# Optimization experiments

Hardware: AMD Instinct MI355X
Metric: run time of the kernel (lower is better)

The kernel has to match this reference:

```python
import jax, jax.numpy as jnp
import numpy as np

IN_DIM, HID_DIM, CNV1_DIM, BATCH = 4096, 2048, 1024, 16384


def setup_inputs() -> dict:
    key = jax.random.key(0)
    ks = jax.random.split(key, 12)
    x = jax.random.normal(ks[0], (BATCH, IN_DIM), dtype=jnp.float32)
    mask_ih = jax.random.randint(ks[1], (HID_DIM, IN_DIM), 0, 2).astype(jnp.bool_)
    mask_hc = jax.random.randint(ks[2], (CNV1_DIM, HID_DIM), 0, 2).astype(jnp.bool_)
    # SparseLinear params (Linear-style: weight [out,in], bias [out])
    lim_ih = 1.0 / np.sqrt(IN_DIM)
    w_ih = jax.random.uniform(ks[3], (HID_DIM, IN_DIM), jnp.float32, -lim_ih, lim_ih)
    b_ih = jax.random.uniform(ks[4], (HID_DIM,), jnp.float32, -lim_ih, lim_ih)
    lim_hc = 1.0 / np.sqrt(HID_DIM)
    w_hc = jax.random.uniform(ks[5], (CNV1_DIM, HID_DIM), jnp.float32, -lim_hc, lim_hc)
    b_hc = jax.random.uniform(ks[6], (CNV1_DIM,), jnp.float32, -lim_hc, lim_hc)
    # Conv1d(1,1,2) weights, kaiming_uniform(tanh): gain=5/3, fan_in=2
    bound = (5.0 / 3.0) * np.sqrt(3.0 / 2.0)
    w_c1 = jax.random.uniform(ks[7], (2,), jnp.float32, -bound, bound)
    w_c2 = jax.random.uniform(ks[8], (2,), jnp.float32, -bound, bound)
    lim_c = 1.0 / np.sqrt(2.0)
    b_c1 = jax.random.uniform(ks[9], (), jnp.float32, -lim_c, lim_c)
    b_c2 = jax.random.uniform(ks[10], (), jnp.float32, -lim_c, lim_c)
    return {"x": x, "mask_ih": mask_ih, "mask_hc": mask_hc,
            "w_ih": w_ih, "b_ih": b_ih, "w_hc": w_hc, "b_hc": b_hc,
            "w_c1": w_c1, "b_c1": b_c1, "w_c2": w_c2, "b_c2": b_c2}


def _conv1d_k2s2(x, w, b):
    # Conv1d(1,1,kernel=2,stride=2) on [B, L] == pairwise reshape + dot
    B, L = x.shape
    return jnp.einsum('blk,k->bl', x.reshape(B, L // 2, 2), w) + b


def reference(x, mask_ih, mask_hc, w_ih, b_ih, w_hc, b_hc, w_c1, b_c1, w_c2, b_c2):
    h = jnp.tanh(x @ (w_ih * mask_ih).T + b_ih)            # [B, HID]
    c = jnp.tanh(h @ (w_hc * mask_hc).T + b_hc)            # [B, CNV1]
    y = jnp.tanh(_conv1d_k2s2(c, w_c1, b_c1))              # [B, CNV1/2]
    y = jnp.tanh(_conv1d_k2s2(y, w_c2, b_c2))              # [B, CNV1/4]
    return y
```

## Files before the change

### kernel.cpp

```cpp
#include <hip/hip_runtime.h>
#include <cstdint>
#include <cstddef>

typedef __bf16  bf16x8f __attribute__((ext_vector_type(8)));
typedef unsigned short u16x8 __attribute__((ext_vector_type(8)));
typedef float   f32x16 __attribute__((ext_vector_type(16)));

__device__ __forceinline__ unsigned short f2bf(float f) {
    union { float f; uint32_t u; } c; c.f = f;
    uint32_t u = c.u;
    return (unsigned short)((u + 0x7fffu + ((u >> 16) & 1u)) >> 16);
}

__device__ __forceinline__ float fast_tanh(float x) {
    float e = __builtin_exp2f(2.885390081777927f * x);
    return 1.0f - 2.0f * __builtin_amdgcn_rcpf(e + 1.0f);
}

__device__ __forceinline__ void load16_lds(const void* g, unsigned short* l) {
    __builtin_amdgcn_global_load_lds(
        (const __attribute__((address_space(1))) unsigned int*)g,
        (__attribute__((address_space(3))) unsigned int*)l,
        16, 0, 0);
}

__global__ __launch_bounds__(256)
void detect_mask(const unsigned char* __restrict__ m, int* __restrict__ flag) {
    __shared__ int s_gt1, s_off;
    if (threadIdx.x == 0) { s_gt1 = 0; s_off = 0; }
    __syncthreads();
    int gt1 = 0, off = 0;
    for (int k = threadIdx.x; k < 4096; k += 256) {
        unsigned char b = m[k];
        if (b > 1) gt1 = 1;
        if ((k & 3) && b) off = 1;
    }
    if (gt1) atomicOr(&s_gt1, 1);
    if (off) atomicOr(&s_off, 1);
    __syncthreads();
    if (threadIdx.x == 0) *flag = (!s_gt1 && s_off) ? 1 : 0;
}

__global__ __launch_bounds__(256)
void cast_f32_bf16(const float* __restrict__ in, unsigned short* __restrict__ out, int n) {
    int tid = blockIdx.x * blockDim.x + threadIdx.x;
    int stride = gridDim.x * blockDim.x;
    for (int e = tid * 4; e < n; e += stride * 4) {
        float4 v = *(const float4*)(in + e);
        ushort4 o;
        o.x = f2bf(v.x); o.y = f2bf(v.y); o.z = f2bf(v.z); o.w = f2bf(v.w);
        *(ushort4*)(out + e) = o;
    }
}

__global__ __launch_bounds__(256)
void mask_cast(const float* __restrict__ w, const void* __restrict__ mv,
               const int* __restrict__ flag, unsigned short* __restrict__ out, int n) {
    const bool u8 = (*flag != 0);
    int tid = blockIdx.x * blockDim.x + threadIdx.x;
    int stride = gridDim.x * blockDim.x;
    for (int e = tid * 4; e < n; e += stride * 4) {
        float4 v = *(const float4*)(w + e);
        int m0, m1, m2, m3;
        if (u8) {
            uchar4 mm = *(const uchar4*)((const unsigned char*)mv + e);
            m0 = mm.x; m1 = mm.y; m2 = mm.z; m3 = mm.w;
        } else {
            int4 mm = ((const int4*)mv)[e >> 2];
            m0 = mm.x; m1 = mm.y; m2 = mm.z; m3 = mm.w;
        }
        ushort4 o;
        o.x = m0 ? f2bf(v.x) : (unsigned short)0;
        o.y = m1 ? f2bf(v.y) : (unsigned short)0;
        o.z = m2 ? f2bf(v.z) : (unsigned short)0;
        o.w = m3 ? f2bf(v.w) : (unsigned short)0;
        *(ushort4*)(out + e) = o;
    }
}

template <typename OutT, bool FUSE>
__global__ __launch_bounds__(512, 2)
void gemm256(const unsigned short* __restrict__ A,
             const unsigned short* __restrict__ W,
             const float* __restrict__ bias,
             OutT* __restrict__ out,
             const float* __restrict__ w1, const float* __restrict__ b1,
             const float* __restrict__ w2, const float* __restrict__ b2,
             int N, int K, int lbx) {
    __shared__ __align__(16) unsigned short lds[65536];

    const int t    = threadIdx.x;
    const int lane = t & 63;
    const int wave = t >> 6;
    const int l31  = lane & 31;
    const int lh   = lane >> 5;
    const int wrow = (wave >> 2) * 128;
    const int wcol = (wave & 3) * 64;

    const int id = blockIdx.x;
    const int bx = id & ((1 << lbx) - 1);
    const int by = id >> lbx;
    const int bm = by * 256, bn = bx * 256;

    const char* Au = (const char*)(A + (size_t)bm * K);
    const char* Wu = (const char*)(W + (size_t)bn * K);

    uint32_t aSrc[2], bSrc[2][2];
#pragma unroll
    for (int j = 0; j < 2; ++j) {
        const int u = t + j * 512;
        { const int r = u >> 2, c = u & 3;
          aSrc[j] = (uint32_t)((r * K + ((c ^ (r & 3)) << 3)) * 2); }
        { const int rl = u >> 3, c = u & 7;
#pragma unroll
          for (int Un = 0; Un < 2; ++Un) {
              const int n = (rl & 31) + ((rl >> 5) << 6) + Un * 32;
              bSrc[Un][j] = (uint32_t)((n * K + ((c ^ (n & 7)) << 3)) * 2);
          } }
    }

    int aRow[4];
#pragma unroll
    for (int mt = 0; mt < 4; ++mt) aRow[mt] = (wrow + mt * 32 + l31) * 32;
    int aSwz[2];
#pragma unroll
    for (int j = 0; j < 2; ++j) aSwz[j] = ((j * 2 + lh) ^ (l31 & 3)) << 3;
    int bBase[2];
#pragma unroll
    for (int nt = 0; nt < 2; ++nt)
        bBase[nt] = 16384 + ((((wcol >> 5) + nt) & 1) * 8192)
                  + (((wcol + nt * 32) >> 6) * 2048) + l31 * 64;
    int bSwz[4];
#pragma unroll
    for (int kp = 0; kp < 2; ++kp)
#pragma unroll
        for (int j = 0; j < 2; ++j)
            bSwz[kp * 2 + j] = ((kp * 4 + j * 2 + lh) ^ (l31 & 7)) << 3;

#define STAGE_A(buf, Uk, kB) do {                                              \
    const char* g_ = Au + (kB);                                                \
    unsigned short* l_ = lds + (buf) * 32768 + (Uk) * 8192 + t * 8;            \
    load16_lds(g_ + aSrc[0] + (Uk) * 64, l_);                                  \
    load16_lds(g_ + aSrc[1] + (Uk) * 64, l_ + 4096);                           \
} while (0)

#define STAGE_B(buf, Un, kB) do {                                              \
    const char* g_ = Wu + (kB);                                                \
    unsigned short* l_ = lds + (buf) * 32768 + 16384 + (Un) * 8192 + t * 8;    \
    load16_lds(g_ + bSrc[Un][0], l_);                                          \
    load16_lds(g_ + bSrc[Un][1], l_ + 4096);                                   \
} while (0)

#define BAR    asm volatile("s_barrier" ::: "memory")
#define VM4BAR do { asm volatile("s_waitcnt vmcnt(4)" ::: "memory"); BAR; } while (0)

#define PHASE(buf, nt, kp, STAGE_STMT) do {                                    \
    u16x8 aF[4][2], bF[2];                                                     \
    const unsigned short* Lb_ = lds + (buf) * 32768;                           \
    _Pragma("unroll")                                                          \
    for (int j_ = 0; j_ < 2; ++j_) {                                           \
        _Pragma("unroll")                                                      \
        for (int mt_ = 0; mt_ < 4; ++mt_)                                      \
            aF[mt_][j_] = *(const u16x8*)(Lb_ + (kp) * 8192 + aRow[mt_] + aSwz[j_]); \
        bF[j_] = *(const u16x8*)(Lb_ + bBase[nt] + bSwz[(kp) * 2 + j_]);       \
    }                                                                          \
    STAGE_STMT;                                                                \
    BAR;                                                                       \
    __builtin_amdgcn_s_setprio(1);                                             \
    _Pragma("unroll")                                                          \
    for (int j_ = 0; j_ < 2; ++j_)                                             \
        _Pragma("unroll")                                                      \
        for (int mt_ = 0; mt_ < 4; ++mt_)                                      \
            acc[mt_][nt] = __builtin_amdgcn_mfma_f32_32x32x16_bf16(            \
                __builtin_bit_cast(bf16x8f, aF[mt_][j_]),                      \
                __builtin_bit_cast(bf16x8f, bF[j_]), acc[mt_][nt], 0, 0, 0);   \
    __builtin_amdgcn_s_setprio(0);                                             \
} while (0)

    f32x16 acc[4][2] = {};

    STAGE_A(0, 0, 0); STAGE_A(0, 1, 0); STAGE_B(0, 0, 0); STAGE_B(0, 1, 0);
    STAGE_A(1, 0, 128); STAGE_B(1, 0, 128);
    asm volatile("s_waitcnt vmcnt(4)" ::: "memory");
    BAR;

    const int KB = K * 2;
    const int KL = KB - 128;
    for (int k0 = 0; k0 < KB; k0 += 256) {
        const int kA = k0 + 128;
        int kB1 = k0 + 256; if (kB1 > KL) kB1 = KL;
        int kB2 = k0 + 384; if (kB2 > KL) kB2 = KL;
        PHASE(0, 0, 0, STAGE_A(1, 1, kA));  BAR;
        PHASE(0, 1, 0, STAGE_B(1, 1, kA));  BAR;
        PHASE(0, 0, 1, STAGE_A(0, 0, kB1)); BAR;
        PHASE(0, 1, 1, STAGE_B(0, 0, kB1)); VM4BAR;
        PHASE(1, 0, 0, STAGE_A(0, 1, kB1)); BAR;
        PHASE(1, 1, 0, STAGE_B(0, 1, kB1)); BAR;
        PHASE(1, 0, 1, STAGE_A(1, 0, kB2)); BAR;
        PHASE(1, 1, 1, STAGE_B(1, 0, kB2)); VM4BAR;
    }
    asm volatile("s_waitcnt vmcnt(0)" ::: "memory");

    float w10 = 0, w11 = 0, bb1 = 0, w20 = 0, w21 = 0, bb2 = 0;
    if constexpr (FUSE) {
        w10 = w1[0]; w11 = w1[1]; bb1 = b1[0];
        w20 = w2[0]; w21 = w2[1]; bb2 = b2[0];
    }
#pragma unroll
    for (int nt = 0; nt < 2; ++nt) {
        const int gn = bn + wcol + nt * 32 + l31;
        const float bv = bias[gn];
#pragma unroll
        for (int mt = 0; mt < 4; ++mt) {
#pragma unroll
            for (int reg = 0; reg < 16; ++reg) {
                const int gm = bm + wrow + mt * 32 + (reg & 3) + 8 * (reg >> 2) + 4 * lh;
                float c = fast_tanh(acc[mt][nt][reg] + bv);
                if constexpr (FUSE) {
                    float c1 = __shfl_xor(c, 1);
                    float c2 = __shfl_xor(c, 2);
                    float c3 = __shfl_xor(c, 3);
                    float y10 = fast_tanh(w10 * c  + w11 * c1 + bb1);
                    float y11 = fast_tanh(w10 * c2 + w11 * c3 + bb1);
                    float y   = fast_tanh(w20 * y10 + w21 * y11 + bb2);
                    if ((lane & 3) == 0)
                        out[(size_t)gm * (N >> 2) + (gn >> 2)] = (OutT)y;
                } else {
                    out[(size_t)gm * N + gn] = (OutT)f2bf(c);
                }
            }
        }
    }
#undef STAGE_A
#undef STAGE_B
#undef BAR
#undef VM4BAR
#undef PHASE
}

extern "C" void kernel_launch(void* const* d_in, const int* in_sizes, int n_in,
                              void* d_out, int out_size, void* d_ws, size_t ws_size,
                              hipStream_t stream) {
    constexpr int B   = 16384;
    constexpr int IN  = 4096;
    constexpr int HID = 2048;
    constexpr int CNV = 1024;

    const float* x       = (const float*)d_in[0];
    const void*  mask_ih = d_in[1];
    const void*  mask_hc = d_in[2];
    const float* w_ih    = (const float*)d_in[3];
    const float* b_ih    = (const float*)d_in[4];
    const float* w_hc    = (const float*)d_in[5];
    const float* b_hc    = (const float*)d_in[6];
    const float* w_c1    = (const float*)d_in[7];
    const float* b_c1    = (const float*)d_in[8];
    const float* w_c2    = (const float*)d_in[9];
    const float* b_c2    = (const float*)d_in[10];
    float* out = (float*)d_out;

    char* ws = (char*)d_ws;
    unsigned short* Xb  = (unsigned short*)(ws);
    unsigned short* Wih = (unsigned short*)(ws + 134217728);
    unsigned short* Whc = (unsigned short*)(ws + 150994944);
    unsigned short* Hb  = (unsigned short*)(ws + 155189248);
    int*            flag = (int*)(ws + 222298112);

    detect_mask<<<1, 256, 0, stream>>>((const unsigned char*)mask_ih, flag);

    cast_f32_bf16<<<4096, 256, 0, stream>>>(x, Xb, B * IN);
    mask_cast<<<1024, 256, 0, stream>>>(w_ih, mask_ih, flag, Wih, HID * IN);
    mask_cast<<<256, 256, 0, stream>>>(w_hc, mask_hc, flag, Whc, CNV * HID);

    gemm256<unsigned short, false><<<512, 512, 0, stream>>>(
        Xb, Wih, b_ih, Hb, nullptr, nullptr, nullptr, nullptr, HID, IN, 3);

    gemm256<float, true><<<256, 512, 0, stream>>>(
        Hb, Whc, b_hc, out, w_c1, b_c1, w_c2, b_c2, CNV, HID, 2);
}
```

Measured before the change: 940.6 us.

## Merge GEMM phases to cover both N-tiles, remap blocks, and change LDS swizzle

Each pipeline phase now loads A fragments once and issues MFMAs for both N sub-tiles, halving the phase count per K step and the redundant A LDS reads. Staging is regrouped two loads per phase with a tighter vmcnt wait. Block IDs are remapped so groups of 8 M-tiles share a column for better L2 reuse of weights. The A-tile LDS swizzle now XORs with (row>>1)&3 to reduce bank conflicts. Fewer barriers, but there is higher register pressure and a less deep prefetch.

```diff
diff --git a/kernel.cpp b/kernel.cpp
--- a/kernel.cpp
+++ b/kernel.cpp
@@ -98,8 +98,8 @@
     const int wcol = (wave & 3) * 64;
 
     const int id = blockIdx.x;
-    const int bx = id & ((1 << lbx) - 1);
-    const int by = id >> lbx;
+    const int bx = (id >> 3) & ((1 << lbx) - 1);
+    const int by = (id & 7) | ((id >> (3 + lbx)) << 3);
     const int bm = by * 256, bn = bx * 256;
 
     const char* Au = (const char*)(A + (size_t)bm * K);
@@ -110,7 +110,7 @@
     for (int j = 0; j < 2; ++j) {
         const int u = t + j * 512;
         { const int r = u >> 2, c = u & 3;
-          aSrc[j] = (uint32_t)((r * K + ((c ^ (r & 3)) << 3)) * 2); }
+          aSrc[j] = (uint32_t)((r * K + ((c ^ ((r >> 1) & 3)) << 3)) * 2); }
         { const int rl = u >> 3, c = u & 7;
 #pragma unroll
           for (int Un = 0; Un < 2; ++Un) {
@@ -124,7 +124,7 @@
     for (int mt = 0; mt < 4; ++mt) aRow[mt] = (wrow + mt * 32 + l31) * 32;
     int aSwz[2];
 #pragma unroll
-    for (int j = 0; j < 2; ++j) aSwz[j] = ((j * 2 + lh) ^ (l31 & 3)) << 3;
+    for (int j = 0; j < 2; ++j) aSwz[j] = ((j * 2 + lh) ^ ((l31 >> 1) & 3)) << 3;
     int bBase[2];
 #pragma unroll
     for (int nt = 0; nt < 2; ++nt)
@@ -152,17 +152,19 @@
 } while (0)
 
 #define BAR    asm volatile("s_barrier" ::: "memory")
-#define VM4BAR do { asm volatile("s_waitcnt vmcnt(4)" ::: "memory"); BAR; } while (0)
-
-#define PHASE(buf, nt, kp, STAGE_STMT) do {                                    \
-    u16x8 aF[4][2], bF[2];                                                     \
+#define VM2BAR do { asm volatile("s_waitcnt vmcnt(2)" ::: "memory"); BAR; } while (0)
+
+#define PHASE(buf, kp, STAGE_STMT) do {                                        \
+    u16x8 aF[4][2], bF[2][2];                                                  \
     const unsigned short* Lb_ = lds + (buf) * 32768;                           \
     _Pragma("unroll")                                                          \
     for (int j_ = 0; j_ < 2; ++j_) {                                           \
         _Pragma("unroll")                                                      \
         for (int mt_ = 0; mt_ < 4; ++mt_)                                      \
             aF[mt_][j_] = *(const u16x8*)(Lb_ + (kp) * 8192 + aRow[mt_] + aSwz[j_]); \
-        bF[j_] = *(const u16x8*)(Lb_ + bBase[nt] + bSwz[(kp) * 2 + j_]);       \
+        _Pragma("unroll")                                                      \
+        for (int nt_ = 0; nt_ < 2; ++nt_)                                      \
+            bF[nt_][j_] = *(const u16x8*)(Lb_ + bBase[nt_] + bSwz[(kp) * 2 + j_]); \
     }                                                                          \
     STAGE_STMT;                                                                \
     BAR;                                                                       \
@@ -171,33 +173,32 @@
     for (int j_ = 0; j_ < 2; ++j_)                                             \
         _Pragma("unroll")                                                      \
         for (int mt_ = 0; mt_ < 4; ++mt_)                                      \
-            acc[mt_][nt] = __builtin_amdgcn_mfma_f32_32x32x16_bf16(            \
-                __builtin_bit_cast(bf16x8f, aF[mt_][j_]),                      \
-                __builtin_bit_cast(bf16x8f, bF[j_]), acc[mt_][nt], 0, 0, 0);   \
+            _Pragma("unroll")                                                  \
+            for (int nt_ = 0; nt_ < 2; ++nt_)                                  \
+                acc[mt_][nt_] = __builtin_amdgcn_mfma_f32_32x32x16_bf16(       \
+                    __builtin_bit_cast(bf16x8f, aF[mt_][j_]),                  \
+                    __builtin_bit_cast(bf16x8f, bF[nt_][j_]),                  \
+                    acc[mt_][nt_], 0, 0, 0);                                   \
     __builtin_amdgcn_s_setprio(0);                                             \
 } while (0)
 
     f32x16 acc[4][2] = {};
 
     STAGE_A(0, 0, 0); STAGE_A(0, 1, 0); STAGE_B(0, 0, 0); STAGE_B(0, 1, 0);
-    STAGE_A(1, 0, 128); STAGE_B(1, 0, 128);
-    asm volatile("s_waitcnt vmcnt(4)" ::: "memory");
+    STAGE_A(1, 0, 128);
+    asm volatile("s_waitcnt vmcnt(2)" ::: "memory");
     BAR;
 
     const int KB = K * 2;
     const int KL = KB - 128;
     for (int k0 = 0; k0 < KB; k0 += 256) {
-        const int kA = k0 + 128;
-        int kB1 = k0 + 256; if (kB1 > KL) kB1 = KL;
-        int kB2 = k0 + 384; if (kB2 > KL) kB2 = KL;
-        PHASE(0, 0, 0, STAGE_A(1, 1, kA));  BAR;
-        PHASE(0, 1, 0, STAGE_B(1, 1, kA));  BAR;
-        PHASE(0, 0, 1, STAGE_A(0, 0, kB1)); BAR;
-        PHASE(0, 1, 1, STAGE_B(0, 0, kB1)); VM4BAR;
-        PHASE(1, 0, 0, STAGE_A(0, 1, kB1)); BAR;
-        PHASE(1, 1, 0, STAGE_B(0, 1, kB1)); BAR;
-        PHASE(1, 0, 1, STAGE_A(1, 0, kB2)); BAR;
-        PHASE(1, 1, 1, STAGE_B(1, 0, kB2)); VM4BAR;
+        const int kO = k0 + 128;
+        int kE2 = k0 + 256; if (kE2 > KL) kE2 = KL;
+        int kO2 = k0 + 384; if (kO2 > KL) kO2 = KL;
+        PHASE(0, 0, STAGE_A(1, 1, kO);  STAGE_B(1, 0, kO));  BAR;
+        PHASE(0, 1, STAGE_B(1, 1, kO);  STAGE_A(0, 0, kE2)); VM2BAR;
+        PHASE(1, 0, STAGE_A(0, 1, kE2); STAGE_B(0, 0, kE2)); BAR;
+        PHASE(1, 1, STAGE_B(0, 1, kE2); STAGE_A(1, 0, kO2)); VM2BAR;
     }
     asm volatile("s_waitcnt vmcnt(0)" ::: "memory");
 
@@ -234,7 +235,7 @@
 #undef STAGE_A
 #undef STAGE_B
 #undef BAR
-#undef VM4BAR
+#undef VM2BAR
 #undef PHASE
 }
 
```

New measurement: 790.2 us. -16.0%, faster.
